# Kernel optimization log

Measured on AMD Instinct MI355X. Metric: run time of the kernel, lower is better.

The kernel has to match this reference:

```python
import jax, jax.numpy as jnp
import numpy as np

N = 10000      # nodes
DEG = 32       # avg degree
D_IN = 256     # in_feats
H = 128        # hidden_layers[0] == hidden_layers[2]
K = 3          # hidden_layers[1] = Chebyshev order
D_OUT = 64     # out_feat


def setup_inputs() -> dict:
    key = jax.random.key(0)
    ks = jax.random.split(key, 8)
    x = jax.random.normal(ks[0], (N, D_IN), jnp.float32)
    # sparse binary adjacency built by scattering into a dense [N, N] matrix
    src = jax.random.randint(ks[1], (N * DEG,), 0, N)
    dst = jax.random.randint(ks[2], (N * DEG,), 0, N)
    adj = jnp.zeros((N, N), jnp.float32).at[src, dst].set(1.0)
    init = lambda k, shape, fan: jax.random.normal(k, shape, jnp.float32) / np.sqrt(fan)
    W_in = init(ks[3], (D_IN, H), D_IN)
    b_in = jnp.zeros((H,), jnp.float32)
    W_cheb = init(ks[4], (K * H, H), K * H)   # dgl ChebConv: Linear(k*in, out)
    b_cheb = jnp.zeros((H,), jnp.float32)
    W_out = init(ks[5], (H, D_OUT), H)
    b_out = jnp.zeros((D_OUT,), jnp.float32)
    return dict(x=x, adj=adj, W_in=W_in, b_in=b_in, W_cheb=W_cheb,
                b_cheb=b_cheb, W_out=W_out, b_out=b_out)


def reference(x, adj, W_in, b_in, W_cheb, b_cheb, W_out, b_out):
    n = x.shape[0]
    # graph construction from dense adjacency (eager, like adj.to_dense().nonzero())
    src, dst = jnp.nonzero(adj)
    # symmetric normalization on in-degrees (dgl ChebConv, norm clamped at 1)
    deg = jax.ops.segment_sum(jnp.ones(src.shape[0], jnp.float32), dst, num_segments=n)
    norm = jnp.clip(deg, 1.0) ** -0.5  # [n]
    re_norm = 2.0 / 2.0  # lambda_max = [2] -> re_norm = 1

    def prop(h):
        # D^{-1/2} A D^{-1/2} h : gather at src, scatter-add at dst
        return jax.ops.segment_sum((h * norm[:, None])[src], dst, num_segments=n) * norm[:, None]

    # input linear + relu
    h = jax.nn.relu(x @ W_in + b_in)
    # Chebyshev recursion (dgl ChebConv with lambda_max=2)
    X0 = h
    X1 = -re_norm * prop(X0) + (re_norm - 1.0) * X0
    Xs = [X0, X1]
    Xpp, Xp = X0, X1
    for _ in range(2, K):
        Xi = -2.0 * re_norm * prop(Xp) + 2.0 * (re_norm - 1.0) * Xp - Xpp
        Xs.append(Xi)
        Xpp, Xp = Xp, Xi
    hc = jax.nn.relu(jnp.concatenate(Xs, axis=1) @ W_cheb + b_cheb)  # [n, H]
    return hc @ W_out + b_out  # [n, D_OUT]
```

## Files before the change

### kernel.cpp

```cpp
#include <hip/hip_runtime.h>
#include <hip/hip_bf16.h>
#include <cstdint>
#include <cstddef>

#define NN 10000
#define MAXDEG 128
#define LDX 384

#define COLSCAN_BLKS 1250
#define RB_ROWS 80
#define NRB 125
#define SEG2 12
#define GEMM_BLKS 313
#define FATG (COLSCAN_BLKS + GEMM_BLKS + 1)

typedef __attribute__((ext_vector_type(8))) short bf16x8;
typedef __attribute__((ext_vector_type(4))) float f32x4;

__device__ __forceinline__ float bf2f(unsigned short u) {
    union { unsigned int i; float f; } c; c.i = ((unsigned int)u) << 16; return c.f;
}
__device__ __forceinline__ unsigned short f2bf(float f) {
    union { float f; unsigned int i; } c; c.f = f;
    unsigned int x = c.i;
    return (unsigned short)((x + 0x7fffu + ((x >> 16) & 1u)) >> 16);
}

__global__ __launch_bounds__(256) void fat_colscan_gemm(
        const float* __restrict__ A,
        int* __restrict__ csr2,
        int* __restrict__ cnt2,
        const float* __restrict__ x, const float* __restrict__ W_in,
        const float* __restrict__ b_in,
        const float* __restrict__ W_cheb, const float* __restrict__ W_out,
        unsigned short* __restrict__ Xc,
        unsigned short* __restrict__ Wtc, unsigned short* __restrict__ Wto) {
    __shared__ float smem[5120];
    int bid = blockIdx.x;
    int t = threadIdx.x;

    if (bid < COLSCAN_BLKS) {
        if (t >= 250) return;
        int rb  = bid / 10;
        int cbs = bid % 10;
        int r0  = rb * RB_ROWS;
        int c   = cbs * 1000 + t * 4;
        const float4* base = (const float4*)A;
        int idx0 = r0 * (NN / 4) + (c >> 2);

        float4 buf[8];
        #pragma unroll
        for (int d = 0; d < 8; ++d)
            buf[d] = base[idx0 + d * (NN / 4)];

        int n0 = 0, n1 = 0, n2 = 0, n3 = 0;
        size_t segbase = ((size_t)rb * NN + c) * SEG2;

        #pragma unroll 8
        for (int r = 0; r < RB_ROWS; ++r) {
            float4 v = buf[r & 7];
            buf[r & 7] = base[idx0 + min(r + 8, RB_ROWS - 1) * (NN / 4)];
            int row = r0 + r;
            if (v.x != 0.f) { if (n0 < SEG2) csr2[segbase + n0] = row; n0++; }
            if (v.y != 0.f) { if (n1 < SEG2) csr2[segbase + SEG2 + n1] = row; n1++; }
            if (v.z != 0.f) { if (n2 < SEG2) csr2[segbase + 2 * SEG2 + n2] = row; n2++; }
            if (v.w != 0.f) { if (n3 < SEG2) csr2[segbase + 3 * SEG2 + n3] = row; n3++; }
        }
        cnt2[(c + 0) * 128 + rb] = n0;
        cnt2[(c + 1) * 128 + rb] = n1;
        cnt2[(c + 2) * 128 + rb] = n2;
        cnt2[(c + 3) * 128 + rb] = n3;
    } else if (bid < COLSCAN_BLKS + GEMM_BLKS) {
        constexpr int K = 256, N = 128, BM = 32, KC = 32;
        float* Wl = smem;
        float* Al = smem + KC * N;
        int r0 = (bid - COLSCAN_BLKS) * BM;
        int c2 = t & 63;
        int g  = t >> 6;
        float2 acc[8];
        #pragma unroll
        for (int i = 0; i < 8; ++i) acc[i] = make_float2(0.f, 0.f);

        for (int kk = 0; kk < K; kk += KC) {
            __syncthreads();
            #pragma unroll
            for (int i = 0; i < KC * N / 4 / 256; ++i) {
                int idx = t + i * 256;
                ((float4*)Wl)[idx] = ((const float4*)(W_in + (size_t)kk * N))[idx];
            }
            {
                int row = t >> 3;
                int cf  = t & 7;
                float4 v = make_float4(0.f, 0.f, 0.f, 0.f);
                if (r0 + row < NN)
                    v = *(const float4*)(x + (size_t)(r0 + row) * K + kk + cf * 4);
                *(float4*)(Al + row * KC + cf * 4) = v;
            }
            __syncthreads();
            for (int k = 0; k < KC; k += 4) {
                float4 av[8];
                #pragma unroll
                for (int rr = 0; rr < 8; ++rr)
                    av[rr] = *(const float4*)(Al + (g * 8 + rr) * KC + k);
                #pragma unroll
                for (int k2 = 0; k2 < 4; ++k2) {
                    float2 wv = *(const float2*)(Wl + (k + k2) * N + c2 * 2);
                    #pragma unroll
                    for (int rr = 0; rr < 8; ++rr) {
                        float a = (k2 == 0) ? av[rr].x : (k2 == 1) ? av[rr].y
                                  : (k2 == 2) ? av[rr].z : av[rr].w;
                        acc[rr].x = fmaf(a, wv.x, acc[rr].x);
                        acc[rr].y = fmaf(a, wv.y, acc[rr].y);
                    }
                }
            }
        }
        float2 bv = *(const float2*)(b_in + c2 * 2);
        #pragma unroll
        for (int rr = 0; rr < 8; ++rr) {
            int r = r0 + g * 8 + rr;
            if (r < NN) {
                float vx = fmaxf(acc[rr].x + bv.x, 0.f);
                float vy = fmaxf(acc[rr].y + bv.y, 0.f);
                uint32_t o = (uint32_t)f2bf(vx) | ((uint32_t)f2bf(vy) << 16);
                *(uint32_t*)(Xc + (size_t)r * LDX + c2 * 2) = o;
            }
        }
    } else {
        for (int idx = t; idx < 384 * 128; idx += 256) {
            int k = idx >> 7, c = idx & 127;
            Wtc[c * 384 + k] = f2bf(W_cheb[idx]);
        }
        for (int idx = t; idx < 128 * 64; idx += 256) {
            int k = idx >> 6, c = idx & 63;
            Wto[c * 128 + k] = f2bf(W_out[idx]);
        }
    }
}

__global__ __launch_bounds__(256) void stitch_norm(
        const int* __restrict__ csr2, const int* __restrict__ cnt2,
        int* __restrict__ csr, int* __restrict__ cnt, float* __restrict__ nrm) {
    int w = threadIdx.x >> 6, l = threadIdx.x & 63;
    int c = blockIdx.x * 4 + w;
    if (c >= NN) return;

    int a  = (l < NRB)      ? cnt2[c * 128 + l]      : 0;
    int bb = (l + 64 < NRB) ? cnt2[c * 128 + 64 + l] : 0;

    int xa = a, xb = bb;
    #pragma unroll
    for (int d = 1; d < 64; d <<= 1) {
        int ya = __shfl_up(xa, d);
        int yb = __shfl_up(xb, d);
        if (l >= d) { xa += ya; xb += yb; }
    }
    int totalA = __shfl(xa, 63);
    int total  = totalA + __shfl(xb, 63);
    int offA = xa - a;
    int offB = totalA + xb - bb;

    const int* segA = csr2 + ((size_t)l * NN + c) * SEG2;
    for (int e = 0; e < a; ++e) {
        int o = offA + e;
        if (o < MAXDEG) csr[(size_t)c * MAXDEG + o] = segA[e];
    }
    if (l + 64 < NRB) {
        const int* segB = csr2 + ((size_t)(l + 64) * NN + c) * SEG2;
        for (int e = 0; e < bb; ++e) {
            int o = offB + e;
            if (o < MAXDEG) csr[(size_t)c * MAXDEG + o] = segB[e];
        }
    }
    if (l == 0) {
        cnt[c] = min(total, MAXDEG);
        nrm[c] = rsqrtf(fmaxf((float)total, 1.f));
    }
}

template<bool SUB>
__global__ __launch_bounds__(256) void prop_k(unsigned short* __restrict__ X,
                                              const int* __restrict__ csr,
                                              const int* __restrict__ cnt,
                                              const float* __restrict__ nrm,
                                              int srcOff, int dstOff, float scale) {
    int j = blockIdx.x * 4 + (threadIdx.x >> 6);
    if (j >= NN) return;
    int lane = threadIdx.x & 63;
    int cn = cnt[j];
    const int* nb = csr + (size_t)j * MAXDEG;
    float ax0 = 0.f, ay0 = 0.f, ax1 = 0.f, ay1 = 0.f;
    float ax2 = 0.f, ay2 = 0.f, ax3 = 0.f, ay3 = 0.f;
    int e = 0;
    for (; e + 4 <= cn; e += 4) {
        int i0 = nb[e], i1 = nb[e + 1], i2 = nb[e + 2], i3 = nb[e + 3];
        float w0 = nrm[i0], w1 = nrm[i1], w2 = nrm[i2], w3 = nrm[i3];
        uint32_t h0 = *(const uint32_t*)(X + (size_t)i0 * LDX + srcOff + lane * 2);
        uint32_t h1 = *(const uint32_t*)(X + (size_t)i1 * LDX + srcOff + lane * 2);
        uint32_t h2 = *(const uint32_t*)(X + (size_t)i2 * LDX + srcOff + lane * 2);
        uint32_t h3 = *(const uint32_t*)(X + (size_t)i3 * LDX + srcOff + lane * 2);
        ax0 = fmaf(w0, bf2f((unsigned short)h0), ax0);
        ay0 = fmaf(w0, bf2f((unsigned short)(h0 >> 16)), ay0);
        ax1 = fmaf(w1, bf2f((unsigned short)h1), ax1);
        ay1 = fmaf(w1, bf2f((unsigned short)(h1 >> 16)), ay1);
        ax2 = fmaf(w2, bf2f((unsigned short)h2), ax2);
        ay2 = fmaf(w2, bf2f((unsigned short)(h2 >> 16)), ay2);
        ax3 = fmaf(w3, bf2f((unsigned short)h3), ax3);
        ay3 = fmaf(w3, bf2f((unsigned short)(h3 >> 16)), ay3);
    }
    for (; e < cn; ++e) {
        int i0 = nb[e];
        float w0 = nrm[i0];
        uint32_t h0 = *(const uint32_t*)(X + (size_t)i0 * LDX + srcOff + lane * 2);
        ax0 = fmaf(w0, bf2f((unsigned short)h0), ax0);
        ay0 = fmaf(w0, bf2f((unsigned short)(h0 >> 16)), ay0);
    }
    float s = scale * nrm[j];
    float rx = s * ((ax0 + ax1) + (ax2 + ax3));
    float ry = s * ((ay0 + ay1) + (ay2 + ay3));
    if (SUB) {
        uint32_t x0 = *(const uint32_t*)(X + (size_t)j * LDX + lane * 2);
        rx -= bf2f((unsigned short)x0);
        ry -= bf2f((unsigned short)(x0 >> 16));
    }
    uint32_t o = (uint32_t)f2bf(rx) | ((uint32_t)f2bf(ry) << 16);
    *(uint32_t*)(X + (size_t)j * LDX + dstOff + lane * 2) = o;
}

__global__ __launch_bounds__(256) void cheb_out_mfma(
        const unsigned short* __restrict__ Xc,
        const unsigned short* __restrict__ Wtc,
        const float* __restrict__ bc,
        const unsigned short* __restrict__ Wto,
        const float* __restrict__ bo,
        float* __restrict__ out) {
    __shared__ unsigned short hcL[32][136];
    int t = threadIdx.x;
    int w = t >> 6, lane = t & 63;
    int r0 = blockIdx.x * 32;
    int lr = lane & 15;
    int kg = lane >> 4;

    f32x4 acc[2][2] = {};
    for (int k0 = 0; k0 < 384; k0 += 32) {
        bf16x8 a[2], b[2];
        #pragma unroll
        for (int m = 0; m < 2; ++m) {
            int row = r0 + m * 16 + lr;
            row = min(row, NN - 1);
            a[m] = *(const bf16x8*)(Xc + (size_t)row * LDX + k0 + kg * 8);
        }
        #pragma unroll
        for (int n = 0; n < 2; ++n) {
            int col = w * 32 + n * 16 + lr;
            b[n] = *(const bf16x8*)(Wtc + (size_t)col * 384 + k0 + kg * 8);
        }
        #pragma unroll
        for (int m = 0; m < 2; ++m)
            #pragma unroll
            for (int n = 0; n < 2; ++n)
                acc[m][n] = __builtin_amdgcn_mfma_f32_16x16x32_bf16(a[m], b[n], acc[m][n], 0, 0, 0);
    }
    #pragma unroll
    for (int m = 0; m < 2; ++m) {
        #pragma unroll
        for (int n = 0; n < 2; ++n) {
            int col = w * 32 + n * 16 + lr;
            float bv = bc[col];
            #pragma unroll
            for (int r = 0; r < 4; ++r) {
                int row = m * 16 + kg * 4 + r;
                hcL[row][col] = f2bf(fmaxf(acc[m][n][r] + bv, 0.f));
            }
        }
    }
    __syncthreads();
    int rt = w >> 1, ch = w & 1;
    f32x4 a2[2] = {};
    for (int k0 = 0; k0 < 128; k0 += 32) {
        bf16x8 af = *(const bf16x8*)(&hcL[rt * 16 + lr][k0 + kg * 8]);
        #pragma unroll
        for (int n = 0; n < 2; ++n) {
            int col = ch * 32 + n * 16 + lr;
            bf16x8 bf_ = *(const bf16x8*)(Wto + (size_t)col * 128 + k0 + kg * 8);
            a2[n] = __builtin_amdgcn_mfma_f32_16x16x32_bf16(af, bf_, a2[n], 0, 0, 0);
        }
    }
    #pragma unroll
    for (int n = 0; n < 2; ++n) {
        int col = ch * 32 + n * 16 + lr;
        float bv = bo[col];
        #pragma unroll
        for (int r = 0; r < 4; ++r) {
            int row = r0 + rt * 16 + kg * 4 + r;
            if (row < NN) out[(size_t)row * 64 + col] = a2[n][r] + bv;
        }
    }
}

extern "C" void kernel_launch(void* const* d_in, const int* in_sizes, int n_in,
                              void* d_out, int out_size, void* d_ws, size_t ws_size,
                              hipStream_t stream) {
    const float* x      = (const float*)d_in[0];
    const float* adj    = (const float*)d_in[1];
    const float* W_in   = (const float*)d_in[2];
    const float* b_in   = (const float*)d_in[3];
    const float* W_cheb = (const float*)d_in[4];
    const float* b_cheb = (const float*)d_in[5];
    const float* W_out  = (const float*)d_in[6];
    const float* b_out  = (const float*)d_in[7];
    float* out = (float*)d_out;

    char* ws = (char*)d_ws;
    int*            cnt  = (int*)(ws + 0);
    float*          nrm  = (float*)(ws + 65536);
    int*            csr  = (int*)(ws + 131072);
    int*            cnt2 = (int*)(ws + 5308416);
    unsigned short* Xc   = (unsigned short*)(ws + 10485760);
    unsigned short* Wtc  = (unsigned short*)(ws + 18874368);
    unsigned short* Wto  = (unsigned short*)(ws + 19005440);
    int*            csr2 = (int*)(ws + 20971520);

    fat_colscan_gemm<<<FATG, 256, 0, stream>>>(
        adj, csr2, cnt2, x, W_in, b_in, W_cheb, W_out, Xc, Wtc, Wto);
    stitch_norm<<<2500, 256, 0, stream>>>(csr2, cnt2, csr, cnt, nrm);
    prop_k<false><<<(NN + 3) / 4, 256, 0, stream>>>(Xc, csr, cnt, nrm, 0, 128, -1.0f);
    prop_k<true><<<(NN + 3) / 4, 256, 0, stream>>>(Xc, csr, cnt, nrm, 128, 256, -2.0f);
    cheb_out_mfma<<<(NN + 31) / 32, 256, 0, stream>>>(Xc, Wtc, b_cheb, Wto, b_out, out);
}
```

Baseline: 234.5 us.

## Fuse CSR stitching with first propagation step via shared-memory neighbor lists

Degree and normalization computation is split into a small separate kernel so that norms for all nodes are ready before stitching. The stitch kernel then keeps each column's neighbor list in shared memory and immediately runs the first Chebyshev propagation (X1 = -prop(X0)) from it. This removes the separate first prop launch and its reload of the CSR rows from global memory. In exchange it adds a launch for the norm kernel, which reads the 128-entry cnt2 rows per node, and a block-wide sync inside the stitch kernel.

```diff
diff --git a/kernel.cpp b/kernel.cpp
--- a/kernel.cpp
+++ b/kernel.cpp
@@ -7,10 +7,10 @@
 #define MAXDEG 128
 #define LDX 384
 
-#define COLSCAN_BLKS 1250
 #define RB_ROWS 80
 #define NRB 125
 #define SEG2 12
+#define COLSCAN_BLKS 1250
 #define GEMM_BLKS 313
 #define FATG (COLSCAN_BLKS + GEMM_BLKS + 1)
 
@@ -26,10 +26,9 @@
     return (unsigned short)((x + 0x7fffu + ((x >> 16) & 1u)) >> 16);
 }
 
-__global__ __launch_bounds__(256) void fat_colscan_gemm(
+__global__ __launch_bounds__(256) void fat_scan_gemm(
         const float* __restrict__ A,
-        int* __restrict__ csr2,
-        int* __restrict__ cnt2,
+        int* __restrict__ csr2, int* __restrict__ cnt2,
         const float* __restrict__ x, const float* __restrict__ W_in,
         const float* __restrict__ b_in,
         const float* __restrict__ W_cheb, const float* __restrict__ W_out,
@@ -138,12 +137,30 @@
     }
 }
 
-__global__ __launch_bounds__(256) void stitch_norm(
+__global__ __launch_bounds__(256) void nrm_k(const int* __restrict__ cnt2,
+                                             int* __restrict__ cnt,
+                                             float* __restrict__ nrm) {
+    int j = blockIdx.x * 256 + threadIdx.x;
+    if (j >= NN) return;
+    const int4* p = (const int4*)(cnt2 + (size_t)j * 128);
+    int s = 0;
+    #pragma unroll
+    for (int k = 0; k < 31; ++k) {
+        int4 v = p[k];
+        s += v.x + v.y + v.z + v.w;
+    }
+    s += cnt2[(size_t)j * 128 + 124];
+    cnt[j] = min(s, MAXDEG);
+    nrm[j] = rsqrtf(fmaxf((float)s, 1.f));
+}
+
+__global__ __launch_bounds__(256) void stitch_prop1(
         const int* __restrict__ csr2, const int* __restrict__ cnt2,
-        int* __restrict__ csr, int* __restrict__ cnt, float* __restrict__ nrm) {
+        const float* __restrict__ nrm,
+        int* __restrict__ csr, unsigned short* __restrict__ X) {
+    __shared__ int nbL[4][MAXDEG];
     int w = threadIdx.x >> 6, l = threadIdx.x & 63;
     int c = blockIdx.x * 4 + w;
-    if (c >= NN) return;
 
     int a  = (l < NRB)      ? cnt2[c * 128 + l]      : 0;
     int bb = (l + 64 < NRB) ? cnt2[c * 128 + 64 + l] : 0;
@@ -163,19 +180,57 @@
     const int* segA = csr2 + ((size_t)l * NN + c) * SEG2;
     for (int e = 0; e < a; ++e) {
         int o = offA + e;
-        if (o < MAXDEG) csr[(size_t)c * MAXDEG + o] = segA[e];
+        if (o < MAXDEG) {
+            int v = segA[e];
+            nbL[w][o] = v;
+            csr[(size_t)c * MAXDEG + o] = v;
+        }
     }
     if (l + 64 < NRB) {
         const int* segB = csr2 + ((size_t)(l + 64) * NN + c) * SEG2;
         for (int e = 0; e < bb; ++e) {
             int o = offB + e;
-            if (o < MAXDEG) csr[(size_t)c * MAXDEG + o] = segB[e];
-        }
-    }
-    if (l == 0) {
-        cnt[c] = min(total, MAXDEG);
-        nrm[c] = rsqrtf(fmaxf((float)total, 1.f));
-    }
+            if (o < MAXDEG) {
+                int v = segB[e];
+                nbL[w][o] = v;
+                csr[(size_t)c * MAXDEG + o] = v;
+            }
+        }
+    }
+    __syncthreads();
+
+    int cn = min(total, MAXDEG);
+    float ax0 = 0.f, ay0 = 0.f, ax1 = 0.f, ay1 = 0.f;
+    float ax2 = 0.f, ay2 = 0.f, ax3 = 0.f, ay3 = 0.f;
+    int e = 0;
+    for (; e + 4 <= cn; e += 4) {
+        int i0 = nbL[w][e], i1 = nbL[w][e + 1], i2 = nbL[w][e + 2], i3 = nbL[w][e + 3];
+        float w0 = nrm[i0], w1 = nrm[i1], w2 = nrm[i2], w3 = nrm[i3];
+        uint32_t h0 = *(const uint32_t*)(X + (size_t)i0 * LDX + l * 2);
+        uint32_t h1 = *(const uint32_t*)(X + (size_t)i1 * LDX + l * 2);
+        uint32_t h2 = *(const uint32_t*)(X + (size_t)i2 * LDX + l * 2);
+        uint32_t h3 = *(const uint32_t*)(X + (size_t)i3 * LDX + l * 2);
+        ax0 = fmaf(w0, bf2f((unsigned short)h0), ax0);
+        ay0 = fmaf(w0, bf2f((unsigned short)(h0 >> 16)), ay0);
+        ax1 = fmaf(w1, bf2f((unsigned short)h1), ax1);
+        ay1 = fmaf(w1, bf2f((unsigned short)(h1 >> 16)), ay1);
+        ax2 = fmaf(w2, bf2f((unsigned short)h2), ax2);
+        ay2 = fmaf(w2, bf2f((unsigned short)(h2 >> 16)), ay2);
+        ax3 = fmaf(w3, bf2f((unsigned short)h3), ax3);
+        ay3 = fmaf(w3, bf2f((unsigned short)(h3 >> 16)), ay3);
+    }
+    for (; e < cn; ++e) {
+        int i0 = nbL[w][e];
+        float w0 = nrm[i0];
+        uint32_t h0 = *(const uint32_t*)(X + (size_t)i0 * LDX + l * 2);
+        ax0 = fmaf(w0, bf2f((unsigned short)h0), ax0);
+        ay0 = fmaf(w0, bf2f((unsigned short)(h0 >> 16)), ay0);
+    }
+    float s = -1.0f * nrm[c];
+    float rx = s * ((ax0 + ax1) + (ax2 + ax3));
+    float ry = s * ((ay0 + ay1) + (ay2 + ay3));
+    uint32_t o = (uint32_t)f2bf(rx) | ((uint32_t)f2bf(ry) << 16);
+    *(uint32_t*)(X + (size_t)c * LDX + 128 + l * 2) = o;
 }
 
 template<bool SUB>
@@ -321,10 +376,10 @@
     unsigned short* Wto  = (unsigned short*)(ws + 19005440);
     int*            csr2 = (int*)(ws + 20971520);
 
-    fat_colscan_gemm<<<FATG, 256, 0, stream>>>(
+    fat_scan_gemm<<<FATG, 256, 0, stream>>>(
         adj, csr2, cnt2, x, W_in, b_in, W_cheb, W_out, Xc, Wtc, Wto);
-    stitch_norm<<<2500, 256, 0, stream>>>(csr2, cnt2, csr, cnt, nrm);
-    prop_k<false><<<(NN + 3) / 4, 256, 0, stream>>>(Xc, csr, cnt, nrm, 0, 128, -1.0f);
+    nrm_k<<<(NN + 255) / 256, 256, 0, stream>>>(cnt2, cnt, nrm);
+    stitch_prop1<<<2500, 256, 0, stream>>>(csr2, cnt2, nrm, csr, Xc);
     prop_k<true><<<(NN + 3) / 4, 256, 0, stream>>>(Xc, csr, cnt, nrm, 128, 256, -2.0f);
     cheb_out_mfma<<<(NN + 31) / 32, 256, 0, stream>>>(Xc, Wtc, b_cheb, Wto, b_out, out);
 }
```

Measured after the change: 236.4 us. About the same (+0.8%).
